# Performance work log

Measured on AMD Instinct MI355X. Metric: run time of the kernel, lower is better.

Reference implementation:

```python
import jax, jax.numpy as jnp
import numpy as np

B, C, H, W = 4, 2048, 32, 32
HID, A, G = 512, 9, 20
SCALE = 32.0
POS_T, NEG_T = 0.7, 0.3
W_CONF, W_REG = 1.0, 5.0
EPS = 1e-8


def _anchor_base():
    # gen_anc_centers + gen_anc_base: centers at (i+0.5); anc_w=scale, anc_h=scale*ratio; clipped to feature-map extent
    scales = jnp.array([2.0, 4.0, 6.0])
    ratios = jnp.array([0.5, 1.0, 1.5])
    aw = jnp.repeat(scales, 3)                       # [A]
    ah = (scales[:, None] * ratios[None, :]).reshape(-1)
    xc = (jnp.arange(W) + 0.5)[None, :, None]        # [1,W,1]
    yc = (jnp.arange(H) + 0.5)[:, None, None]        # [H,1,1]
    x1 = jnp.clip(xc - aw / 2, 0.0, W)
    y1 = jnp.clip(yc - ah / 2, 0.0, H)
    x2 = jnp.clip(xc + aw / 2, 0.0, W)
    y2 = jnp.clip(yc + ah / 2, 0.0, H)
    anc = jnp.stack(jnp.broadcast_arrays(x1, y1, x2, y2), axis=-1)  # [H,W,A,4]
    return anc.reshape(-1, 4)                        # [N,4], N = H*W*A


def _conv(x, w, b):
    y = jax.lax.conv_general_dilated(x, w, (1, 1), 'SAME',
                                     dimension_numbers=('NCHW', 'OIHW', 'NCHW'))
    return y + b[None, :, None, None]


def setup_inputs():
    key = jax.random.key(0)
    ks = jax.random.split(key, 8)
    feature_map = jax.random.normal(ks[0], (B, C, H, W), jnp.float32)
    # valid GT boxes in pixel coords of a 1024x1024 image
    ctr = jax.random.uniform(ks[1], (B, G, 2), minval=0.15, maxval=0.85) * 1024.0
    wh = jax.random.uniform(ks[2], (B, G, 2), minval=0.05, maxval=0.30) * 1024.0
    gt_bboxes = jnp.clip(jnp.concatenate([ctr - wh / 2, ctr + wh / 2], -1), 0.0, 1024.0)
    gt_classes = jax.random.randint(ks[3], (B, G), 1, 21)
    f1 = 1.0 / np.sqrt(C * 9)
    f2 = 1.0 / np.sqrt(HID)
    conv1_w = jax.random.uniform(ks[4], (HID, C, 3, 3), jnp.float32, -f1, f1)
    conv1_b = jnp.zeros((HID,), jnp.float32)
    conf_w = jax.random.uniform(ks[5], (A, HID, 1, 1), jnp.float32, -f2, f2)
    conf_b = jnp.zeros((A,), jnp.float32)
    reg_w = jax.random.uniform(ks[6], (A * 4, HID, 1, 1), jnp.float32, -f2, f2)
    reg_b = jnp.zeros((A * 4,), jnp.float32)
    return {"feature_map": feature_map, "gt_bboxes": gt_bboxes, "gt_classes": gt_classes,
            "conv1_w": conv1_w, "conv1_b": conv1_b, "conf_w": conf_w, "conf_b": conf_b,
            "reg_w": reg_w, "reg_b": reg_b}


def reference(feature_map, gt_bboxes, gt_classes, conv1_w, conv1_b, conf_w, conf_b, reg_w, reg_b):
    # ProposalModule (dropout = eval identity)
    hid = jax.nn.relu(_conv(feature_map, conv1_w, conv1_b))
    conf = _conv(hid, conf_w, conf_b).transpose(0, 2, 3, 1).reshape(B, -1)       # [B,N]
    offs = _conv(hid, reg_w, reg_b).transpose(0, 2, 3, 1).reshape(B, -1, 4)      # [B,N,4]

    anc = _anchor_base()                              # [N,4]
    gt = gt_bboxes / SCALE                            # project_bboxes p2a

    # IoU [B,N,G]
    lt = jnp.maximum(anc[None, :, None, :2], gt[:, None, :, :2])
    rb = jnp.minimum(anc[None, :, None, 2:], gt[:, None, :, 2:])
    inter = jnp.clip(rb - lt, 0.0).prod(-1)
    area_a = (anc[:, 2] - anc[:, 0]) * (anc[:, 3] - anc[:, 1])
    area_g = (gt[..., 2] - gt[..., 0]) * (gt[..., 3] - gt[..., 1])
    iou = inter / (area_a[None, :, None] + area_g[:, None, :] - inter + EPS)

    # positive: IoU > pos_thresh OR best anchor for each GT; negative: max IoU < neg_thresh
    max_per_gt = iou.max(axis=1, keepdims=True)
    pos = ((iou > POS_T) | ((iou == max_per_gt) & (max_per_gt > EPS))).any(-1)    # [B,N]
    max_per_anc = iou.max(-1)
    gi = iou.argmax(-1)                               # assigned GT per anchor
    neg = (max_per_anc < NEG_T) & (~pos)

    assigned = jnp.take_along_axis(gt, jnp.broadcast_to(gi[:, :, None], gi.shape + (4,)), axis=1)

    acx = (anc[:, 0] + anc[:, 2]) / 2; acy = (anc[:, 1] + anc[:, 3]) / 2
    aw_ = anc[:, 2] - anc[:, 0];       ah_ = anc[:, 3] - anc[:, 1]
    gcx = (assigned[..., 0] + assigned[..., 2]) / 2; gcy = (assigned[..., 1] + assigned[..., 3]) / 2
    gw = assigned[..., 2] - assigned[..., 0];        gh = assigned[..., 3] - assigned[..., 1]
    gt_off = jnp.stack([(gcx - acx) / (aw_ + EPS), (gcy - acy) / (ah_ + EPS),
                        jnp.log((gw + EPS) / (aw_ + EPS)), jnp.log((gh + EPS) / (ah_ + EPS))], -1)

    posf = pos.astype(conf.dtype)
    negf = neg.astype(conf.dtype)
    # BCE-with-logits, reduction='sum' / batch_size (pos target 1, neg target 0)
    cls_loss = ((jax.nn.softplus(-conf) * posf).sum() + (jax.nn.softplus(conf) * negf).sum()) / B
    d = offs - gt_off
    sl1 = jnp.where(jnp.abs(d) < 1.0, 0.5 * d * d, jnp.abs(d) - 0.5)
    reg_loss = (sl1 * posf[..., None]).sum() / B
    total = W_CONF * cls_loss + W_REG * reg_loss

    # generate_proposals from positive anchors + predicted offsets (mask instead of gather for jit)
    pcx = acx + offs[..., 0] * aw_; pcy = acy + offs[..., 1] * ah_
    pw = aw_ * jnp.exp(offs[..., 2]); ph = ah_ * jnp.exp(offs[..., 3])
    proposals = jnp.stack([pcx - pw / 2, pcy - ph / 2, pcx + pw / 2, pcy + ph / 2], -1)
    proposals = proposals * posf[..., None]
    return total, proposals, pos
```

## Files before the change

### kernel.cpp

```cpp
#include <hip/hip_runtime.h>


typedef __bf16 bf16x8 __attribute__((ext_vector_type(8)));
typedef float floatx4 __attribute__((ext_vector_type(4)));

#define NB 4
#define NC 2048
#define NH 32
#define NW 32
#define NHID 512
#define NA 9
#define NG 20
#define NANC 9216
#define NM 4096

#define OFF_XH    0ull
#define OFF_WT    18939904ull
#define OFF_WH    37814272ull
#define OFF_HB    37863424ull
#define OFF_MAXG  37863680ull
#define OFF_SUMS  37864192ull
#define OFF_CTR   37864320ull
#define OFF_HIDP  37864448ull

#define PREP_TX   4096
#define PREP_W    4096
#define PREP_WH   96
#define PREP_HALO 528
#define PREP_MAXG 80
#define PREP_NBLK (PREP_TX + PREP_W + PREP_WH + PREP_HALO + PREP_MAXG + 1)

__device__ __forceinline__ unsigned short f2bf(float f) {
  unsigned int u = __float_as_uint(f);
  u = (u + 0x7fffu + ((u >> 16) & 1u)) >> 16;
  return (unsigned short)u;
}

__device__ __forceinline__ void gload16(const void* g, void* l) {
  __builtin_amdgcn_global_load_lds(
      (const __attribute__((address_space(1))) unsigned int*)g,
      (__attribute__((address_space(3))) unsigned int*)l, 16, 0, 0);
}

__constant__ float c_aw[9] = {2.f,2.f,2.f,4.f,4.f,4.f,6.f,6.f,6.f};
__constant__ float c_ah[9] = {1.f,2.f,3.f,2.f,4.f,6.f,3.f,6.f,9.f};

struct Anc { float x1, y1, x2, y2, areaA; };
__device__ __forceinline__ Anc anc_of(int n) {
  const int a = n % 9, pix = n / 9;
  const int xi = pix & 31, yi = pix >> 5;
  const float hw = c_aw[a]*0.5f, hh = c_ah[a]*0.5f;
  const float xc = xi + 0.5f, yc = yi + 0.5f;
  Anc A;
  A.x1 = fminf(fmaxf(xc - hw, 0.f), 32.f);
  A.y1 = fminf(fmaxf(yc - hh, 0.f), 32.f);
  A.x2 = fminf(fmaxf(xc + hw, 0.f), 32.f);
  A.y2 = fminf(fmaxf(yc + hh, 0.f), 32.f);
  A.areaA = __fmul_rn(__fsub_rn(A.x2, A.x1), __fsub_rn(A.y2, A.y1));
  return A;
}
__device__ __forceinline__ float iou_one(const Anc& A, float4 gp) {
  const float gx1 = gp.x * 0.03125f, gy1 = gp.y * 0.03125f;
  const float gx2 = gp.z * 0.03125f, gy2 = gp.w * 0.03125f;
  const float dx = fmaxf(__fsub_rn(fminf(A.x2, gx2), fmaxf(A.x1, gx1)), 0.f);
  const float dy = fmaxf(__fsub_rn(fminf(A.y2, gy2), fmaxf(A.y1, gy1)), 0.f);
  const float inter = __fmul_rn(dx, dy);
  const float areaG = __fmul_rn(__fsub_rn(gx2, gx1), __fsub_rn(gy2, gy1));
  const float den = __fadd_rn(__fsub_rn(__fadd_rn(A.areaA, areaG), inter), 1e-8f);
  return __fdiv_rn(inter, den);
}

__global__ __launch_bounds__(256) void k_prep(const float* __restrict__ x,
                                              const float* __restrict__ w1,
                                              const float* __restrict__ cw, const float* __restrict__ cb,
                                              const float* __restrict__ rw, const float* __restrict__ rb,
                                              const float* __restrict__ gtb,
                                              unsigned short* __restrict__ xh,
                                              unsigned short* __restrict__ wt,
                                              unsigned short* __restrict__ wh, float* __restrict__ hb,
                                              unsigned int* __restrict__ maxg,
                                              float* __restrict__ sums, unsigned int* __restrict__ ctr) {
  __shared__ float tile[64][33];
  __shared__ float red[4];
  const int bid = blockIdx.x;
  const int tid = threadIdx.x;

  if (bid < PREP_TX) {
    const int c0 = (bid & 31) << 6;
    const int h  = (bid >> 5) & 31;
    const int b  = bid >> 10;
    const int w = tid & 31, cl = tid >> 5;
    const float* src = x + (((size_t)b*NC + c0)*NH + h)*NW;
#pragma unroll
    for (int j = 0; j < 8; ++j) {
      const int c = cl + j*8;
      tile[c][w] = src[(size_t)c*NH*NW + w];
    }
    __syncthreads();
    unsigned short* dst = xh + ((size_t)(b*34 + h + 1)*34 + 1)*2048 + c0;
    const int w2 = tid >> 3, c8 = (tid & 7) << 3;
    unsigned int pk[4];
#pragma unroll
    for (int k = 0; k < 4; ++k) {
      const unsigned int lo = f2bf(tile[c8 + 2*k][w2]);
      const unsigned int hi = f2bf(tile[c8 + 2*k + 1][w2]);
      pk[k] = lo | (hi << 16);
    }
    *(uint4*)(dst + (size_t)w2*2048 + c8) = make_uint4(pk[0], pk[1], pk[2], pk[3]);
    return;
  }
  if (bid < PREP_TX + PREP_W) {
    const int t = (bid - PREP_TX)*256 + tid;
    const float* src = w1 + (size_t)t * 9;
#pragma unroll
    for (int g = 0; g < 9; ++g)
      wt[(size_t)g*NHID*NC + t] = f2bf(src[g]);
    return;
  }
  if (bid < PREP_TX + PREP_W + PREP_WH) {
    const int t = (bid - PREP_TX - PREP_W)*256 + tid;
    const int n = t >> 9, c = t & 511;
    float v = 0.f;
    if (n < 9) v = cw[n*512 + c];
    else if (n < 45) v = rw[(n-9)*512 + c];
    wh[t] = f2bf(v);
    if (c == 0) {
      float bv = 0.f;
      if (n < 9) bv = cb[n];
      else if (n < 45) bv = rb[n-9];
      hb[n] = bv;
    }
    return;
  }
  if (bid < PREP_TX + PREP_W + PREP_WH + PREP_HALO) {
    const int q = bid - (PREP_TX + PREP_W + PREP_WH);
    const int b = q / 132, hc = q - b*132;
    int hh, ww;
    if (hc < 34)       { hh = 0;        ww = hc; }
    else if (hc < 68)  { hh = 33;       ww = hc - 34; }
    else if (hc < 100) { hh = hc - 67;  ww = 0; }
    else               { hh = hc - 99;  ww = 33; }
    uint4* dst = (uint4*)(xh + ((size_t)((b*34 + hh)*34 + ww))*2048);
    dst[tid] = make_uint4(0u, 0u, 0u, 0u);
    return;
  }
  if (bid < PREP_TX + PREP_W + PREP_WH + PREP_HALO + PREP_MAXG) {
    const int p = bid - (PREP_TX + PREP_W + PREP_WH + PREP_HALO);
    const int b = p / NG, g = p - b*NG;
    const float4 gp = *(const float4*)(gtb + ((size_t)b*NG + g)*4);
    float m = 0.f;
#pragma unroll
    for (int j = 0; j < 36; ++j)
      m = fmaxf(m, iou_one(anc_of(tid + j*256), gp));
#pragma unroll
    for (int o = 32; o > 0; o >>= 1) m = fmaxf(m, __shfl_xor(m, o));
    if ((tid & 63) == 0) red[tid >> 6] = m;
    __syncthreads();
    if (tid == 0)
      maxg[b*NG + g] = __float_as_uint(fmaxf(fmaxf(red[0], red[1]), fmaxf(red[2], red[3])));
    return;
  }
  if (tid < 2) sums[tid] = 0.f;
  else if (tid == 2) *ctr = 0u;
}

__global__ __launch_bounds__(256, 4) void k_conv_gemm(const unsigned short* __restrict__ xh,
                                                      const unsigned short* __restrict__ wt,
                                                      unsigned short* __restrict__ hidp,
                                                      int csplit, int ksh) {
  __shared__ unsigned short As[128*64] __attribute__((aligned(16)));
  __shared__ unsigned short Bs[128*64] __attribute__((aligned(16)));
  const int t = threadIdx.x;
  const int L = blockIdx.x;
  const int kz = L & ((1 << ksh) - 1);
  const int rem = L >> ksh;
  const int tileM = rem & 31, tileN = rem >> 5;
  const int b = tileM >> 3, h0 = (tileM & 7) << 2;
  const int o0 = tileN << 7;
  const int wv = t >> 6, lane = t & 63;
  const int wm = wv >> 1, wn = wv & 1;
  const int quad = lane >> 4, l16 = lane & 15;
  const int c_base = kz * csplit;

  floatx4 acc[4][4];
#pragma unroll
  for (int mt = 0; mt < 4; ++mt)
#pragma unroll
    for (int nt = 0; nt < 4; ++nt)
      acc[mt][nt] = (floatx4){0.f, 0.f, 0.f, 0.f};

  const int lr = lane >> 3, pos = lane & 7;
  int gA[4], gB[4];
#pragma unroll
  for (int j = 0; j < 4; ++j) {
    const int row = wv*32 + j*8 + lr;
    const int sd = (pos - row) & 7;
    const int hh = h0 + (row >> 5) + 1, ww = (row & 31) + 1;
    gA[j] = ((b*34 + hh)*34 + ww)*2048 + c_base + sd*8;
    gB[j] = (o0 + row)*2048 + c_base + sd*8;
  }

  for (int g = 0; g < 9; ++g) {
    const int dsp = ((g/3 - 1)*34 + (g%3 - 1)) * 2048;
    const unsigned short* wgp = wt + (size_t)g*NHID*NC;
    for (int c0 = 0; c0 < csplit; c0 += 64) {
#pragma unroll
      for (int j = 0; j < 4; ++j) {
        gload16(xh + gA[j] + dsp + c0, As + (wv*32 + j*8)*64);
        gload16(wgp + gB[j] + c0,      Bs + (wv*32 + j*8)*64);
      }
      __syncthreads();
#pragma unroll
      for (int sub = 0; sub < 2; ++sub) {
        const int ps = ((sub*4 + quad) + l16) & 7;
        bf16x8 af[4], bw[4];
#pragma unroll
        for (int mt = 0; mt < 4; ++mt)
          af[mt] = *(const bf16x8*)(As + (wm*64 + mt*16 + l16)*64 + ps*8);
#pragma unroll
        for (int nt = 0; nt < 4; ++nt)
          bw[nt] = *(const bf16x8*)(Bs + (wn*64 + nt*16 + l16)*64 + ps*8);
#pragma unroll
        for (int mt = 0; mt < 4; ++mt)
#pragma unroll
          for (int nt = 0; nt < 4; ++nt)
            acc[mt][nt] = __builtin_amdgcn_mfma_f32_16x16x32_bf16(af[mt], bw[nt], acc[mt][nt], 0, 0, 0);
      }
      __syncthreads();
    }
  }
  unsigned short* hp = hidp + (size_t)kz*NM*NHID;
#pragma unroll
  for (int mt = 0; mt < 4; ++mt) {
    const int m = tileM*128 + wm*64 + mt*16 + quad*4;
#pragma unroll
    for (int nt = 0; nt < 4; ++nt) {
      const int o = o0 + wn*64 + nt*16 + l16;
#pragma unroll
      for (int r = 0; r < 4; ++r)
        hp[(size_t)(m + r)*NHID + o] = f2bf(acc[mt][nt][r]);
    }
  }
}

__device__ __forceinline__ float softplusf(float z) {
  return fmaxf(z, 0.f) + log1pf(expf(-fabsf(z)));
}
__device__ __forceinline__ float sl1f(float d) {
  const float ad = fabsf(d);
  return ad < 1.f ? 0.5f*d*d : ad - 0.5f;
}

__global__ __launch_bounds__(256) void k_heads_assign(const unsigned short* __restrict__ hidp,
                                                      const float* __restrict__ b1,
                                                      const unsigned short* __restrict__ wh,
                                                      const float* __restrict__ hb,
                                                      const float* __restrict__ gtb,
                                                      const unsigned int* __restrict__ maxg,
                                                      float* __restrict__ out,
                                                      float* __restrict__ sums,
                                                      unsigned int* __restrict__ ctr,
                                                      int nsplit) {
  __shared__ unsigned short As[64*40] __attribute__((aligned(16)));
  __shared__ unsigned short Bs[48*40] __attribute__((aligned(16)));
  __shared__ float hl[64][49];
  __shared__ float4 gt_s[20];
  __shared__ float  mg_s[20];
  const int t = threadIdx.x;
  const int tile = blockIdx.x;
  const int b = tile >> 4, pix0 = (tile & 15) << 6;

  if (t < 20) {
    gt_s[t] = *(const float4*)(gtb + ((size_t)b*NG + t)*4);
    mg_s[t] = __uint_as_float(maxg[b*NG + t]);
  }

  const int wv = t >> 6, lane = t & 63;
  const int quad = lane >> 4, l16 = lane & 15;
  floatx4 acc[3];
#pragma unroll
  for (int nt = 0; nt < 3; ++nt) acc[nt] = (floatx4){0.f, 0.f, 0.f, 0.f};
  const int row0 = t >> 2, seg = t & 3;
  for (int c0 = 0; c0 < 512; c0 += 32) {
    {
      const size_t gi = ((size_t)(tile*64 + row0))*512 + c0 + seg*8;
      float s[8] = {0.f,0.f,0.f,0.f,0.f,0.f,0.f,0.f};
      for (int sp = 0; sp < nsplit; ++sp) {
        const uint4 v = *(const uint4*)(hidp + (size_t)sp*NM*NHID + gi);
        s[0] += __uint_as_float(v.x << 16); s[1] += __uint_as_float(v.x & 0xffff0000u);
        s[2] += __uint_as_float(v.y << 16); s[3] += __uint_as_float(v.y & 0xffff0000u);
        s[4] += __uint_as_float(v.z << 16); s[5] += __uint_as_float(v.z & 0xffff0000u);
        s[6] += __uint_as_float(v.w << 16); s[7] += __uint_as_float(v.w & 0xffff0000u);
      }
      const int cb0 = c0 + seg*8;
      unsigned int pk[4];
#pragma unroll
      for (int k = 0; k < 4; ++k) {
        const unsigned int lo = f2bf(fmaxf(s[2*k]   + b1[cb0 + 2*k],     0.f));
        const unsigned int hi = f2bf(fmaxf(s[2*k+1] + b1[cb0 + 2*k + 1], 0.f));
        pk[k] = lo | (hi << 16);
      }
      *(uint4*)(As + row0*40 + seg*8) = make_uint4(pk[0], pk[1], pk[2], pk[3]);
    }
    if (t < 192)
      *(uint4*)(Bs + row0*40 + seg*8) =
          *(const uint4*)(wh + (size_t)row0*512 + c0 + seg*8);
    __syncthreads();
    const bf16x8 af = *(const bf16x8*)(As + (wv*16 + l16)*40 + quad*8);
#pragma unroll
    for (int nt = 0; nt < 3; ++nt) {
      const bf16x8 bw = *(const bf16x8*)(Bs + (nt*16 + l16)*40 + quad*8);
      acc[nt] = __builtin_amdgcn_mfma_f32_16x16x32_bf16(af, bw, acc[nt], 0, 0, 0);
    }
    __syncthreads();
  }
#pragma unroll
  for (int nt = 0; nt < 3; ++nt) {
    const int nn = nt*16 + l16;
    const float bv = hb[nn];
#pragma unroll
    for (int r = 0; r < 4; ++r)
      hl[wv*16 + quad*4 + r][nn] = acc[nt][r] + bv;
  }
  __syncthreads();

  float cs = 0.f, rs = 0.f;
#pragma unroll
  for (int k = 0; k < 3; ++k) {
    const int q = t + k*256;
    if (q < 576) {
      const int pixL = q / 9, a = q - pixL*9;
      const int pix = pix0 + pixL;
      const int n = pix*9 + a;
      const int idx = b*NANC + n;
      const Anc A = anc_of(n);

      float mx = -1.f; int gi = 0; bool pos = false;
      for (int g = 0; g < NG; ++g) {
        const float v = iou_one(A, gt_s[g]);
        const float mg = mg_s[g];
        pos = pos || (v > 0.7f) || ((v == mg) && (mg > 1e-8f));
        if (v > mx) { mx = v; gi = g; }
      }
      const bool neg = (mx < 0.3f) && !pos;
      const float posf = pos ? 1.f : 0.f;

      const float conf = hl[pixL][a];
      const float of0 = hl[pixL][9 + a*4 + 0];
      const float of1 = hl[pixL][9 + a*4 + 1];
      const float of2 = hl[pixL][9 + a*4 + 2];
      const float of3 = hl[pixL][9 + a*4 + 3];

      if (pos) cs += softplusf(-conf);
      else if (neg) cs += softplusf(conf);

      const float acx = (A.x1 + A.x2)*0.5f, acy = (A.y1 + A.y2)*0.5f;
      const float aw = A.x2 - A.x1, ah = A.y2 - A.y1;
      if (pos) {
        const float4 gp = gt_s[gi];
        const float gx1 = gp.x*0.03125f, gy1 = gp.y*0.03125f;
        const float gx2 = gp.z*0.03125f, gy2 = gp.w*0.03125f;
        const float gcx = (gx1+gx2)*0.5f, gcy = (gy1+gy2)*0.5f;
        const float gw = gx2-gx1, gh = gy2-gy1;
        const float t0 = (gcx-acx)/(aw+1e-8f), t1 = (gcy-acy)/(ah+1e-8f);
        const float t2 = logf((gw+1e-8f)/(aw+1e-8f)), t3 = logf((gh+1e-8f)/(ah+1e-8f));
        rs += sl1f(of0-t0) + sl1f(of1-t1) + sl1f(of2-t2) + sl1f(of3-t3);
      }

      const float pcx = acx + of0*aw, pcy = acy + of1*ah;
      const float pw = aw*expf(of2), ph = ah*expf(of3);
      float* op = out + 1 + (size_t)idx*4;
      op[0] = (pcx - pw*0.5f)*posf;
      op[1] = (pcy - ph*0.5f)*posf;
      op[2] = (pcx + pw*0.5f)*posf;
      op[3] = (pcy + ph*0.5f)*posf;
      out[1 + 4*(size_t)NB*NANC + idx] = posf;
    }
  }
#pragma unroll
  for (int o = 32; o > 0; o >>= 1) { cs += __shfl_xor(cs, o); rs += __shfl_xor(rs, o); }
  if ((t & 63) == 0) { atomicAdd(&sums[0], cs); atomicAdd(&sums[1], rs); }

  __syncthreads();
  if (t == 0) {
    __threadfence();
    const unsigned int c = atomicAdd(ctr, 1u);
    if (c == 63u) {
      __threadfence();
      const float fcs = atomicAdd(&sums[0], 0.f);
      const float frs = atomicAdd(&sums[1], 0.f);
      out[0] = fcs*0.25f + 5.f*(frs*0.25f);
    }
  }
}

extern "C" void kernel_launch(void* const* d_in, const int* in_sizes, int n_in,
                              void* d_out, int out_size, void* d_ws, size_t ws_size,
                              hipStream_t stream) {
  const float* x   = (const float*)d_in[0];
  const float* gtb = (const float*)d_in[1];
  const float* w1  = (const float*)d_in[3];
  const float* b1  = (const float*)d_in[4];
  const float* cw  = (const float*)d_in[5];
  const float* cb  = (const float*)d_in[6];
  const float* rw  = (const float*)d_in[7];
  const float* rb  = (const float*)d_in[8];
  float* out = (float*)d_out;
  char* ws = (char*)d_ws;

  unsigned short* xh    = (unsigned short*)(ws + OFF_XH);
  unsigned short* wt    = (unsigned short*)(ws + OFF_WT);
  unsigned short* wh    = (unsigned short*)(ws + OFF_WH);
  float*          hb    = (float*)(ws + OFF_HB);
  unsigned int*   maxg  = (unsigned int*)(ws + OFF_MAXG);
  float*          sums  = (float*)(ws + OFF_SUMS);
  unsigned int*   ctr   = (unsigned int*)(ws + OFF_CTR);
  unsigned short* hidp  = (unsigned short*)(ws + OFF_HIDP);

  int nsplit = 8, ksh = 3;
  while (nsplit > 1 && OFF_HIDP + (size_t)nsplit*NM*NHID*2 > ws_size) { nsplit >>= 1; --ksh; }
  const int csplit = NC / nsplit;

  k_prep<<<PREP_NBLK, 256, 0, stream>>>(x, w1, cw, cb, rw, rb, gtb, xh, wt, wh, hb, maxg, sums, ctr);
  k_conv_gemm<<<128*nsplit, 256, 0, stream>>>(xh, wt, hidp, csplit, ksh);
  k_heads_assign<<<64, 256, 0, stream>>>(hidp, b1, wh, hb, gtb, maxg, out, sums, ctr, nsplit);
}
```

Before: 246.0 us.

## Split heads kernel into 256 blocks with K-split reduction and coalesce weight transpose

The heads/assignment kernel now runs 256 blocks of 16 pixels instead of 64 blocks of 64 pixels. Each of the four waves handles a quarter of the 512 hidden channels, and the partial MFMA accumulators are summed through shared memory. This removes the per-step LDS staging and barriers and gives the GPU more blocks to spread the small kernel across CUs. Separately, the conv weight transpose-to-bf16 prep now uses float4 coalesced reads and transposes through LDS, so writes go out as 16-byte vectors instead of strided scalar stores. The cost is a larger LDS footprint in the prep kernel (an 18 KB buffer), which can lower occupancy for the other prep branches.

New measurement: 226.4 us (median of 2 runs). 8.0% less time.

```diff
diff --git a/kernel.cpp b/kernel.cpp
--- a/kernel.cpp
+++ b/kernel.cpp
@@ -24,7 +24,7 @@
 #define OFF_HIDP  37864448ull
 
 #define PREP_TX   4096
-#define PREP_W    4096
+#define PREP_W    1024
 #define PREP_WH   96
 #define PREP_HALO 528
 #define PREP_MAXG 80
@@ -81,6 +81,7 @@
                                               unsigned int* __restrict__ maxg,
                                               float* __restrict__ sums, unsigned int* __restrict__ ctr) {
   __shared__ float tile[64][33];
+  __shared__ unsigned short wlds[9*1024];
   __shared__ float red[4];
   const int bid = blockIdx.x;
   const int tid = threadIdx.x;
@@ -110,11 +111,32 @@
     return;
   }
   if (bid < PREP_TX + PREP_W) {
-    const int t = (bid - PREP_TX)*256 + tid;
-    const float* src = w1 + (size_t)t * 9;
-#pragma unroll
-    for (int g = 0; g < 9; ++g)
-      wt[(size_t)g*NHID*NC + t] = f2bf(src[g]);
+    const int p = bid - PREP_TX;
+    const int o = p >> 1, half = p & 1;
+    const int c_base = half << 10;
+    const float* src = w1 + ((size_t)(o*2048 + c_base))*9;
+#pragma unroll
+    for (int j = 0; j < 9; ++j) {
+      const int f0 = (j*256 + tid)*4;
+      const float4 v = *(const float4*)(src + f0);
+      const float vv[4] = {v.x, v.y, v.z, v.w};
+#pragma unroll
+      for (int e = 0; e < 4; ++e) {
+        const int f = f0 + e;
+        const int c = f/9, g = f - c*9;
+        wlds[g*1024 + c] = f2bf(vv[e]);
+      }
+    }
+    __syncthreads();
+#pragma unroll
+    for (int j = 0; j < 5; ++j) {
+      const int idx = j*256 + tid;
+      if (idx < 1152) {
+        const int g = idx >> 7, off = (idx & 127) << 3;
+        *(uint4*)(wt + (size_t)g*NHID*NC + o*2048 + c_base + off) =
+            *(const uint4*)(wlds + g*1024 + off);
+      }
+    }
     return;
   }
   if (bid < PREP_TX + PREP_W + PREP_WH) {
@@ -261,14 +283,13 @@
                                                       float* __restrict__ sums,
                                                       unsigned int* __restrict__ ctr,
                                                       int nsplit) {
-  __shared__ unsigned short As[64*40] __attribute__((aligned(16)));
-  __shared__ unsigned short Bs[48*40] __attribute__((aligned(16)));
-  __shared__ float hl[64][49];
+  __shared__ float red[4][16][48];
+  __shared__ float hl[16][49];
   __shared__ float4 gt_s[20];
   __shared__ float  mg_s[20];
   const int t = threadIdx.x;
-  const int tile = blockIdx.x;
-  const int b = tile >> 4, pix0 = (tile & 15) << 6;
+  const int bid = blockIdx.x;
+  const int b = bid >> 6, pix0 = (bid & 63) << 4;
 
   if (t < 20) {
     gt_s[t] = *(const float4*)(gtb + ((size_t)b*NG + t)*4);
@@ -280,102 +301,92 @@
   floatx4 acc[3];
 #pragma unroll
   for (int nt = 0; nt < 3; ++nt) acc[nt] = (floatx4){0.f, 0.f, 0.f, 0.f};
-  const int row0 = t >> 2, seg = t & 3;
-  for (int c0 = 0; c0 < 512; c0 += 32) {
-    {
-      const size_t gi = ((size_t)(tile*64 + row0))*512 + c0 + seg*8;
-      float s[8] = {0.f,0.f,0.f,0.f,0.f,0.f,0.f,0.f};
-      for (int sp = 0; sp < nsplit; ++sp) {
-        const uint4 v = *(const uint4*)(hidp + (size_t)sp*NM*NHID + gi);
-        s[0] += __uint_as_float(v.x << 16); s[1] += __uint_as_float(v.x & 0xffff0000u);
-        s[2] += __uint_as_float(v.y << 16); s[3] += __uint_as_float(v.y & 0xffff0000u);
-        s[4] += __uint_as_float(v.z << 16); s[5] += __uint_as_float(v.z & 0xffff0000u);
-        s[6] += __uint_as_float(v.w << 16); s[7] += __uint_as_float(v.w & 0xffff0000u);
-      }
-      const int cb0 = c0 + seg*8;
-      unsigned int pk[4];
-#pragma unroll
-      for (int k = 0; k < 4; ++k) {
-        const unsigned int lo = f2bf(fmaxf(s[2*k]   + b1[cb0 + 2*k],     0.f));
-        const unsigned int hi = f2bf(fmaxf(s[2*k+1] + b1[cb0 + 2*k + 1], 0.f));
-        pk[k] = lo | (hi << 16);
-      }
-      *(uint4*)(As + row0*40 + seg*8) = make_uint4(pk[0], pk[1], pk[2], pk[3]);
-    }
-    if (t < 192)
-      *(uint4*)(Bs + row0*40 + seg*8) =
-          *(const uint4*)(wh + (size_t)row0*512 + c0 + seg*8);
-    __syncthreads();
-    const bf16x8 af = *(const bf16x8*)(As + (wv*16 + l16)*40 + quad*8);
+
+  const int m = bid*16 + l16;
+#pragma unroll
+  for (int kk = 0; kk < 4; ++kk) {
+    const int ch0 = wv*128 + kk*32 + quad*8;
+    float s[8] = {0.f,0.f,0.f,0.f,0.f,0.f,0.f,0.f};
+    const size_t gi = (size_t)m*NHID + ch0;
+    for (int sp = 0; sp < nsplit; ++sp) {
+      const uint4 v = *(const uint4*)(hidp + (size_t)sp*NM*NHID + gi);
+      s[0] += __uint_as_float(v.x << 16); s[1] += __uint_as_float(v.x & 0xffff0000u);
+      s[2] += __uint_as_float(v.y << 16); s[3] += __uint_as_float(v.y & 0xffff0000u);
+      s[4] += __uint_as_float(v.z << 16); s[5] += __uint_as_float(v.z & 0xffff0000u);
+      s[6] += __uint_as_float(v.w << 16); s[7] += __uint_as_float(v.w & 0xffff0000u);
+    }
+    union { unsigned short u[8]; bf16x8 v; } af;
+#pragma unroll
+    for (int e = 0; e < 8; ++e)
+      af.u[e] = f2bf(fmaxf(s[e] + b1[ch0 + e], 0.f));
 #pragma unroll
     for (int nt = 0; nt < 3; ++nt) {
-      const bf16x8 bw = *(const bf16x8*)(Bs + (nt*16 + l16)*40 + quad*8);
-      acc[nt] = __builtin_amdgcn_mfma_f32_16x16x32_bf16(af, bw, acc[nt], 0, 0, 0);
-    }
-    __syncthreads();
-  }
-#pragma unroll
-  for (int nt = 0; nt < 3; ++nt) {
-    const int nn = nt*16 + l16;
-    const float bv = hb[nn];
+      const bf16x8 bf = *(const bf16x8*)(wh + (size_t)(nt*16 + l16)*NHID + ch0);
+      acc[nt] = __builtin_amdgcn_mfma_f32_16x16x32_bf16(af.v, bf, acc[nt], 0, 0, 0);
+    }
+  }
+#pragma unroll
+  for (int nt = 0; nt < 3; ++nt)
 #pragma unroll
     for (int r = 0; r < 4; ++r)
-      hl[wv*16 + quad*4 + r][nn] = acc[nt][r] + bv;
-  }
+      red[wv][quad*4 + r][nt*16 + l16] = acc[nt][r];
   __syncthreads();
+#pragma unroll
+  for (int j = 0; j < 3; ++j) {
+    const int idx = t + j*256;
+    const int i = idx / 48, c = idx - i*48;
+    hl[i][c] = red[0][i][c] + red[1][i][c] + red[2][i][c] + red[3][i][c] + hb[c];
+  }
+  __syncthreads();
 
   float cs = 0.f, rs = 0.f;
-#pragma unroll
-  for (int k = 0; k < 3; ++k) {
-    const int q = t + k*256;
-    if (q < 576) {
-      const int pixL = q / 9, a = q - pixL*9;
-      const int pix = pix0 + pixL;
-      const int n = pix*9 + a;
-      const int idx = b*NANC + n;
-      const Anc A = anc_of(n);
-
-      float mx = -1.f; int gi = 0; bool pos = false;
-      for (int g = 0; g < NG; ++g) {
-        const float v = iou_one(A, gt_s[g]);
-        const float mg = mg_s[g];
-        pos = pos || (v > 0.7f) || ((v == mg) && (mg > 1e-8f));
-        if (v > mx) { mx = v; gi = g; }
-      }
-      const bool neg = (mx < 0.3f) && !pos;
-      const float posf = pos ? 1.f : 0.f;
-
-      const float conf = hl[pixL][a];
-      const float of0 = hl[pixL][9 + a*4 + 0];
-      const float of1 = hl[pixL][9 + a*4 + 1];
-      const float of2 = hl[pixL][9 + a*4 + 2];
-      const float of3 = hl[pixL][9 + a*4 + 3];
-
-      if (pos) cs += softplusf(-conf);
-      else if (neg) cs += softplusf(conf);
-
-      const float acx = (A.x1 + A.x2)*0.5f, acy = (A.y1 + A.y2)*0.5f;
-      const float aw = A.x2 - A.x1, ah = A.y2 - A.y1;
-      if (pos) {
-        const float4 gp = gt_s[gi];
-        const float gx1 = gp.x*0.03125f, gy1 = gp.y*0.03125f;
-        const float gx2 = gp.z*0.03125f, gy2 = gp.w*0.03125f;
-        const float gcx = (gx1+gx2)*0.5f, gcy = (gy1+gy2)*0.5f;
-        const float gw = gx2-gx1, gh = gy2-gy1;
-        const float t0 = (gcx-acx)/(aw+1e-8f), t1 = (gcy-acy)/(ah+1e-8f);
-        const float t2 = logf((gw+1e-8f)/(aw+1e-8f)), t3 = logf((gh+1e-8f)/(ah+1e-8f));
-        rs += sl1f(of0-t0) + sl1f(of1-t1) + sl1f(of2-t2) + sl1f(of3-t3);
-      }
-
-      const float pcx = acx + of0*aw, pcy = acy + of1*ah;
-      const float pw = aw*expf(of2), ph = ah*expf(of3);
-      float* op = out + 1 + (size_t)idx*4;
-      op[0] = (pcx - pw*0.5f)*posf;
-      op[1] = (pcy - ph*0.5f)*posf;
-      op[2] = (pcx + pw*0.5f)*posf;
-      op[3] = (pcy + ph*0.5f)*posf;
-      out[1 + 4*(size_t)NB*NANC + idx] = posf;
-    }
+  if (t < 144) {
+    const int pixL = t / 9, a = t - pixL*9;
+    const int pix = pix0 + pixL;
+    const int n = pix*9 + a;
+    const int idx = b*NANC + n;
+    const Anc A = anc_of(n);
+
+    float mx = -1.f; int gi = 0; bool pos = false;
+    for (int g = 0; g < NG; ++g) {
+      const float v = iou_one(A, gt_s[g]);
+      const float mg = mg_s[g];
+      pos = pos || (v > 0.7f) || ((v == mg) && (mg > 1e-8f));
+      if (v > mx) { mx = v; gi = g; }
+    }
+    const bool neg = (mx < 0.3f) && !pos;
+    const float posf = pos ? 1.f : 0.f;
+
+    const float conf = hl[pixL][a];
+    const float of0 = hl[pixL][9 + a*4 + 0];
+    const float of1 = hl[pixL][9 + a*4 + 1];
+    const float of2 = hl[pixL][9 + a*4 + 2];
+    const float of3 = hl[pixL][9 + a*4 + 3];
+
+    if (pos) cs = softplusf(-conf);
+    else if (neg) cs = softplusf(conf);
+
+    const float acx = (A.x1 + A.x2)*0.5f, acy = (A.y1 + A.y2)*0.5f;
+    const float aw = A.x2 - A.x1, ah = A.y2 - A.y1;
+    if (pos) {
+      const float4 gp = gt_s[gi];
+      const float gx1 = gp.x*0.03125f, gy1 = gp.y*0.03125f;
+      const float gx2 = gp.z*0.03125f, gy2 = gp.w*0.03125f;
+      const float gcx = (gx1+gx2)*0.5f, gcy = (gy1+gy2)*0.5f;
+      const float gw = gx2-gx1, gh = gy2-gy1;
+      const float t0 = (gcx-acx)/(aw+1e-8f), t1 = (gcy-acy)/(ah+1e-8f);
+      const float t2 = logf((gw+1e-8f)/(aw+1e-8f)), t3 = logf((gh+1e-8f)/(ah+1e-8f));
+      rs = sl1f(of0-t0) + sl1f(of1-t1) + sl1f(of2-t2) + sl1f(of3-t3);
+    }
+
+    const float pcx = acx + of0*aw, pcy = acy + of1*ah;
+    const float pw = aw*expf(of2), ph = ah*expf(of3);
+    float* op = out + 1 + (size_t)idx*4;
+    op[0] = (pcx - pw*0.5f)*posf;
+    op[1] = (pcy - ph*0.5f)*posf;
+    op[2] = (pcx + pw*0.5f)*posf;
+    op[3] = (pcy + ph*0.5f)*posf;
+    out[1 + 4*(size_t)NB*NANC + idx] = posf;
   }
 #pragma unroll
   for (int o = 32; o > 0; o >>= 1) { cs += __shfl_xor(cs, o); rs += __shfl_xor(rs, o); }
@@ -385,7 +396,7 @@
   if (t == 0) {
     __threadfence();
     const unsigned int c = atomicAdd(ctr, 1u);
-    if (c == 63u) {
+    if (c == 255u) {
       __threadfence();
       const float fcs = atomicAdd(&sums[0], 0.f);
       const float frs = atomicAdd(&sums[1], 0.f);
@@ -423,5 +434,5 @@
 
   k_prep<<<PREP_NBLK, 256, 0, stream>>>(x, w1, cw, cb, rw, rb, gtb, xh, wt, wh, hb, maxg, sums, ctr);
   k_conv_gemm<<<128*nsplit, 256, 0, stream>>>(xh, wt, hidp, csplit, ksh);
-  k_heads_assign<<<64, 256, 0, stream>>>(hidp, b1, wh, hb, gtb, maxg, out, sums, ctr, nsplit);
-}
+  k_heads_assign<<<256, 256, 0, stream>>>(hidp, b1, wh, hb, gtb, maxg, out, sums, ctr, nsplit);
+}
```
